# Performance work log

Measured on AMD Instinct MI355X. Metric: run time of the kernel, lower is better.

The kernel has to match this reference:

```python
import jax, jax.numpy as jnp
import numpy as np

SHIFT = 1  # module picks random +-1 at init; fixed deterministically to +1


def setup_inputs() -> dict:
    key = jax.random.key(0)
    k1, k2, k3 = jax.random.split(key, 3)
    x = jax.random.normal(k1, (128, 128, 56, 56), dtype=jnp.float32)
    w0 = jax.random.normal(k2, (2, 3, 3, 32), dtype=jnp.float32)
    w1 = jax.random.normal(k3, (64, 4), dtype=jnp.float32)
    return {"x": x, "w0": w0, "w1": w1}


def _unfold3(t, axis):
    # F.unfold with kernel (3,1), padding (1,0) along `axis` (length 56):
    # zero-pad by 1 on each side, then stack the 3 shifted windows as a new
    # axis placed just BEFORE `axis` (matching torch's C*kh channel ordering
    # after the reshapes in the original module).
    pad = [(0, 0)] * t.ndim
    pad[axis] = (1, 1)
    p = jnp.pad(t, pad)
    slices = []
    for a in range(3):
        idx = [slice(None)] * t.ndim
        idx[axis] = slice(a, a + 56)
        slices.append(p[tuple(idx)])
    return jnp.stack(slices, axis=axis)


def reference(x, w0, w1):
    # x: (128,128,56,56) -> (k=128, j=64, m=2, n=56, l=56)
    t3 = x.reshape(128, 64, 2, 56, 56)
    # channel mix: contract j=64 against w1 (64,4) -> (b, m=2, n=56, l=56, i=4)
    t4 = jnp.einsum('kjmnl,ji->kmnli', t3, w1)
    # first unfold over l (axis 3): (b, 2, 56, kA=3, l=56, i=4)
    u1 = _unfold3(t4, axis=3)
    # second unfold over l again (now axis 4), padding applied to u1 (which
    # already contains zeros from the first padding) -> (b,2,56,kA,kB,l,i)
    u2 = _unfold3(u1, axis=4)
    # torch permute (0,1,2,5,4,3,6): (b, 2, 56, l, kB, kA, i)
    t5 = jnp.transpose(u2, (0, 1, 2, 5, 4, 3, 6))
    # conv-like contraction with w0 (l=2, i=3, k=3, j=32) -> (b,56,56,4,32)
    t6 = jnp.einsum('mlonikp,likj->monpj', t5, w0)
    # (b,56,56,32,4) -> (b,56,56,128), roll along H, -> NCHW
    t7 = jnp.transpose(t6, (0, 1, 2, 4, 3)).reshape(128, 56, 56, 128)
    t7 = jnp.roll(t7, SHIFT, axis=1)
    return jnp.transpose(t7, (0, 3, 1, 2))
```

## Files before the change

kernel.cpp:

```cpp
#include <hip/hip_runtime.h>

namespace {
constexpr int HH = 56, WW = 56;
constexpr int CPLANE = HH * WW;

__global__ __launch_bounds__(448, 1) void chanmix_kernel(
    const float* __restrict__ x,
    const float* __restrict__ w1,
    float* __restrict__ t4g)
{
    __shared__ float4 w1s[64];
    const int tid = threadIdx.x;
    if (tid < 64) w1s[tid] = ((const float4*)w1)[tid];
    __syncthreads();

    const int b  = blockIdx.x >> 1;
    const int h0 = (blockIdx.x & 1) * 28;
    if (tid >= 392) return;

    const int rh = tid / 14;
    const int w0 = (tid - rh * 14) * 4;
    const float* xp = x + ((size_t)b * 128 * HH + (h0 + rh)) * WW + w0;

    float acc[2][4][4] = {};

    for (int c0 = 0; c0 < 128; c0 += 8) {
        float4 xv[8];
        #pragma unroll
        for (int k = 0; k < 8; ++k)
            xv[k] = *(const float4*)(xp + (size_t)(c0 + k) * CPLANE);
        #pragma unroll
        for (int k = 0; k < 8; ++k) {
            const int m = k & 1;
            const float4 wv = w1s[(c0 + k) >> 1];
            const float xk[4] = {xv[k].x, xv[k].y, xv[k].z, xv[k].w};
            const float wk[4] = {wv.x, wv.y, wv.z, wv.w};
            #pragma unroll
            for (int i = 0; i < 4; ++i)
                #pragma unroll
                for (int q = 0; q < 4; ++q)
                    acc[m][i][q] = fmaf(xk[q], wk[i], acc[m][i][q]);
        }
    }

    float* tp = t4g + (size_t)(b * HH + h0 + rh) * 448 + w0;
    #pragma unroll
    for (int m = 0; m < 2; ++m)
        #pragma unroll
        for (int i = 0; i < 4; ++i)
            *(float4*)(tp + (m * 4 + i) * WW) =
                make_float4(acc[m][i][0], acc[m][i][1], acc[m][i][2], acc[m][i][3]);
}

__global__ __launch_bounds__(256, 2) void conv_kernel(
    const float* __restrict__ t4g,
    const float* __restrict__ w0,
    float* __restrict__ out)
{
    __shared__ float ls[14][8][60];
    __shared__ float Wc[32][2][5];
    __shared__ float fx0[32][2], fx3[32][2];

    const int tid = threadIdx.x;
    const int b   = blockIdx.x >> 2;
    const int h0  = (blockIdx.x & 3) * 14;

    if (tid < 64) {
        const int j = tid >> 1, m = tid & 1;
        float w[3][3];
        #pragma unroll
        for (int kB = 0; kB < 3; ++kB)
            #pragma unroll
            for (int kA = 0; kA < 3; ++kA)
                w[kB][kA] = w0[((m * 3 + kB) * 3 + kA) * 32 + j];
        Wc[j][m][0] = w[0][0];
        Wc[j][m][1] = w[0][1] + w[1][0];
        Wc[j][m][2] = w[0][2] + w[1][1] + w[2][0];
        Wc[j][m][3] = w[1][2] + w[2][1];
        Wc[j][m][4] = w[2][2];
        fx0[j][m] = w[0][2];
        fx3[j][m] = w[2][0];
    }

    if (tid < 224) {
        const int row  = tid >> 1;
        const int half = tid & 1;
        *(float2*)&ls[row >> 3][row & 7][half ? 58 : 0] = make_float2(0.f, 0.f);
    }

    const float4* src = (const float4*)(t4g + (size_t)(b * HH + h0) * 448);
    #pragma unroll
    for (int k = 0; k < 7; ++k) {
        const int idx = k * 256 + tid;
        if (idx < 1568) {
            const float4 v = src[idx];
            const int row = idx / 14, wq = idx - row * 14;
            float* d = &ls[row >> 3][row & 7][2 + 4 * wq];
            *(float2*)d       = make_float2(v.x, v.y);
            *(float2*)(d + 2) = make_float2(v.z, v.w);
        }
    }
    __syncthreads();

    if (tid >= 196) return;
    const int rh = tid / 14;
    const int wq = tid - rh * 14;
    const int l0 = 4 * wq;

    float v[2][4][8];
    #pragma unroll
    for (int m = 0; m < 2; ++m)
        #pragma unroll
        for (int i = 0; i < 4; ++i) {
            const float* p = &ls[rh][m * 4 + i][l0];
            const float4 p0 = *(const float4*)p;
            const float4 p1 = *(const float4*)(p + 4);
            v[m][i][0] = p0.x; v[m][i][1] = p0.y; v[m][i][2] = p0.z; v[m][i][3] = p0.w;
            v[m][i][4] = p1.x; v[m][i][5] = p1.y; v[m][i][6] = p1.z; v[m][i][7] = p1.w;
        }

    const int h_out = (h0 + rh + 1) % HH;
    float* obase = out + ((size_t)b * 128 * HH + h_out) * WW + l0;

    #pragma unroll 2
    for (int j = 0; j < 32; ++j) {
        float W[2][5], f0[2], f3[2];
        #pragma unroll
        for (int m = 0; m < 2; ++m) {
            #pragma unroll
            for (int d = 0; d < 5; ++d) W[m][d] = Wc[j][m][d];
            f0[m] = fx0[j][m];
            f3[m] = fx3[j][m];
        }
        #pragma unroll
        for (int i = 0; i < 4; ++i) {
            float o0 = 0.f, o1 = 0.f, o2 = 0.f, o3 = 0.f;
            #pragma unroll
            for (int m = 0; m < 2; ++m)
                #pragma unroll
                for (int d = 0; d < 5; ++d) {
                    const float wd = W[m][d];
                    o0 = fmaf(v[m][i][d],     wd, o0);
                    o1 = fmaf(v[m][i][d + 1], wd, o1);
                    o2 = fmaf(v[m][i][d + 2], wd, o2);
                    o3 = fmaf(v[m][i][d + 3], wd, o3);
                }
            if (wq == 0)  o0 -= v[0][i][2] * f0[0] + v[1][i][2] * f0[1];
            if (wq == 13) o3 -= v[0][i][5] * f3[0] + v[1][i][5] * f3[1];
            *(float4*)(obase + (size_t)(j * 4 + i) * CPLANE) = make_float4(o0, o1, o2, o3);
        }
    }
}
}

extern "C" void kernel_launch(void* const* d_in, const int* in_sizes, int n_in,
                              void* d_out, int out_size, void* d_ws, size_t ws_size,
                              hipStream_t stream) {
    const float* x  = (const float*)d_in[0];
    const float* w0 = (const float*)d_in[1];
    const float* w1 = (const float*)d_in[2];
    float* out = (float*)d_out;
    float* t4g = (float*)d_ws;

    chanmix_kernel<<<dim3(128 * 2), dim3(448), 0, stream>>>(x, w1, t4g);
    conv_kernel<<<dim3(128 * 4), dim3(256), 0, stream>>>(t4g, w0, out);
}
```

Measured before the change: 142.1 us.

## Fuse channel-mix and conv kernels, keeping intermediate in shared memory

Merges the channel-mix kernel into the conv kernel. Each block computes its 14-row slice of the channel-mixed intermediate directly into shared memory instead of writing it to a global workspace and reading it back. The channel loop is also double-buffered in registers so the next 8-channel loads are issued before the current FMAs. This removes a second launch and the global round trip for the intermediate, at the cost of higher register pressure and only 196 of 256 threads doing work in the x-reading phase. The ls array gains an unused row dimension.

```diff
diff --git a/kernel.cpp b/kernel.cpp
--- a/kernel.cpp
+++ b/kernel.cpp
@@ -4,69 +4,25 @@
 constexpr int HH = 56, WW = 56;
 constexpr int CPLANE = HH * WW;
 
-__global__ __launch_bounds__(448, 1) void chanmix_kernel(
+__global__ __launch_bounds__(256, 2) void fused_kernel(
     const float* __restrict__ x,
+    const float* __restrict__ w0,
     const float* __restrict__ w1,
-    float* __restrict__ t4g)
-{
-    __shared__ float4 w1s[64];
-    const int tid = threadIdx.x;
-    if (tid < 64) w1s[tid] = ((const float4*)w1)[tid];
-    __syncthreads();
-
-    const int b  = blockIdx.x >> 1;
-    const int h0 = (blockIdx.x & 1) * 28;
-    if (tid >= 392) return;
-
-    const int rh = tid / 14;
-    const int w0 = (tid - rh * 14) * 4;
-    const float* xp = x + ((size_t)b * 128 * HH + (h0 + rh)) * WW + w0;
-
-    float acc[2][4][4] = {};
-
-    for (int c0 = 0; c0 < 128; c0 += 8) {
-        float4 xv[8];
-        #pragma unroll
-        for (int k = 0; k < 8; ++k)
-            xv[k] = *(const float4*)(xp + (size_t)(c0 + k) * CPLANE);
-        #pragma unroll
-        for (int k = 0; k < 8; ++k) {
-            const int m = k & 1;
-            const float4 wv = w1s[(c0 + k) >> 1];
-            const float xk[4] = {xv[k].x, xv[k].y, xv[k].z, xv[k].w};
-            const float wk[4] = {wv.x, wv.y, wv.z, wv.w};
-            #pragma unroll
-            for (int i = 0; i < 4; ++i)
-                #pragma unroll
-                for (int q = 0; q < 4; ++q)
-                    acc[m][i][q] = fmaf(xk[q], wk[i], acc[m][i][q]);
-        }
-    }
-
-    float* tp = t4g + (size_t)(b * HH + h0 + rh) * 448 + w0;
-    #pragma unroll
-    for (int m = 0; m < 2; ++m)
-        #pragma unroll
-        for (int i = 0; i < 4; ++i)
-            *(float4*)(tp + (m * 4 + i) * WW) =
-                make_float4(acc[m][i][0], acc[m][i][1], acc[m][i][2], acc[m][i][3]);
-}
-
-__global__ __launch_bounds__(256, 2) void conv_kernel(
-    const float* __restrict__ t4g,
-    const float* __restrict__ w0,
     float* __restrict__ out)
 {
-    __shared__ float ls[14][8][60];
-    __shared__ float Wc[32][2][5];
-    __shared__ float fx0[32][2], fx3[32][2];
+    __shared__ float  ls[14][9][60];
+    __shared__ float  Wc[32][2][5];
+    __shared__ float  fx0[32][2], fx3[32][2];
+    __shared__ float4 w1s[64];
 
     const int tid = threadIdx.x;
     const int b   = blockIdx.x >> 2;
     const int h0  = (blockIdx.x & 3) * 14;
 
-    if (tid < 64) {
-        const int j = tid >> 1, m = tid & 1;
+    if (tid < 64) w1s[tid] = ((const float4*)w1)[tid];
+
+    if (tid >= 64 && tid < 128) {
+        const int j = (tid - 64) >> 1, m = (tid - 64) & 1;
         float w[3][3];
         #pragma unroll
         for (int kB = 0; kB < 3; ++kB)
@@ -88,24 +44,61 @@
         *(float2*)&ls[row >> 3][row & 7][half ? 58 : 0] = make_float2(0.f, 0.f);
     }
 
-    const float4* src = (const float4*)(t4g + (size_t)(b * HH + h0) * 448);
-    #pragma unroll
-    for (int k = 0; k < 7; ++k) {
-        const int idx = k * 256 + tid;
-        if (idx < 1568) {
-            const float4 v = src[idx];
-            const int row = idx / 14, wq = idx - row * 14;
-            float* d = &ls[row >> 3][row & 7][2 + 4 * wq];
-            *(float2*)d       = make_float2(v.x, v.y);
-            *(float2*)(d + 2) = make_float2(v.z, v.w);
+    __syncthreads();
+
+    const int  rh = tid / 14;
+    const int  wq = tid - rh * 14;
+    const int  l0 = 4 * wq;
+    const bool active = (tid < 196);
+
+    if (active) {
+        const float* xp = x + ((size_t)b * 128 * HH + (h0 + rh)) * WW + l0;
+        float acc[2][4][4] = {};
+        float4 pA[8], pB[8];
+
+        auto LOADG = [&](float4* buf, int c0) {
+            #pragma unroll
+            for (int k = 0; k < 8; ++k)
+                buf[k] = *(const float4*)(xp + (size_t)(c0 + k) * CPLANE);
+        };
+        auto FMA8 = [&](const float4* buf, int c0) {
+            #pragma unroll
+            for (int k = 0; k < 8; ++k) {
+                const int m = k & 1;
+                const float4 wv = w1s[(c0 + k) >> 1];
+                const float xk[4] = {buf[k].x, buf[k].y, buf[k].z, buf[k].w};
+                const float wk[4] = {wv.x, wv.y, wv.z, wv.w};
+                #pragma unroll
+                for (int i = 0; i < 4; ++i)
+                    #pragma unroll
+                    for (int q = 0; q < 4; ++q)
+                        acc[m][i][q] = fmaf(xk[q], wk[i], acc[m][i][q]);
+            }
+        };
+
+        LOADG(pA, 0);
+        #pragma unroll
+        for (int c0 = 0; c0 < 112; c0 += 16) {
+            LOADG(pB, c0 + 8);
+            FMA8(pA, c0);
+            LOADG(pA, c0 + 16);
+            FMA8(pB, c0 + 8);
         }
+        LOADG(pB, 120);
+        FMA8(pA, 112);
+        FMA8(pB, 120);
+
+        #pragma unroll
+        for (int m = 0; m < 2; ++m)
+            #pragma unroll
+            for (int i = 0; i < 4; ++i) {
+                *(float2*)&ls[rh][m * 4 + i][2 + l0]     = make_float2(acc[m][i][0], acc[m][i][1]);
+                *(float2*)&ls[rh][m * 4 + i][2 + l0 + 2] = make_float2(acc[m][i][2], acc[m][i][3]);
+            }
     }
     __syncthreads();
 
-    if (tid >= 196) return;
-    const int rh = tid / 14;
-    const int wq = tid - rh * 14;
-    const int l0 = 4 * wq;
+    if (!active) return;
 
     float v[2][4][8];
     #pragma unroll
@@ -160,8 +153,5 @@
     const float* w0 = (const float*)d_in[1];
     const float* w1 = (const float*)d_in[2];
     float* out = (float*)d_out;
-    float* t4g = (float*)d_ws;
-
-    chanmix_kernel<<<dim3(128 * 2), dim3(448), 0, stream>>>(x, w1, t4g);
-    conv_kernel<<<dim3(128 * 4), dim3(256), 0, stream>>>(t4g, w0, out);
+    fused_kernel<<<dim3(128 * 4), dim3(256), 0, stream>>>(x, w0, w1, out);
 }
```

Measured after the change: 131.0 us. 7.8% less time.
